# Kernel optimization log

Measured on AMD Instinct MI355X. Metric: run time of the kernel, lower is better.

## Reference

```python
import jax, jax.numpy as jnp
import numpy as np
from jax import lax

N, C, M = 512, 81, 28
NMS_THRESH = 0.5
EPS = 1e-4


def setup_inputs() -> dict:
    key = jax.random.key(0)
    k1, k2, k3, k4 = jax.random.split(key, 4)
    return {
        "left_logits": jax.random.normal(k1, (N, C, M, M), dtype=jnp.float32),
        "right_logits": jax.random.normal(k2, (N, C, M, M), dtype=jnp.float32),
        "scores": jax.random.uniform(k3, (N,), dtype=jnp.float32),
        "labels": jax.random.randint(k4, (N,), 0, C),
    }


def mask_nms_keep(probs, scores, thresh):
    # probs: [N, M, M] float mask probabilities; greedy suppression in score order.
    n = probs.shape[0]
    order = jnp.argsort(-scores)
    P = probs[order].reshape(n, -1)                  # [N, M*M] sorted by score desc
    inter = P @ P.T                                   # pairwise sum(mask_i * mask_j)
    u = P.sum(-1)                                     # per-mask area (numerator mask only)
    iou = inter / (u[:, None] + EPS)                  # asymmetric IoU as in mask_iou()
    upper = jnp.triu(jnp.ones((n, n), dtype=bool), 1) # j > i

    def body(i, suppressed):
        sup_row = (~suppressed[i]) & upper[i] & (iou[i] >= thresh)
        return suppressed | sup_row

    suppressed = lax.fori_loop(0, n, body, jnp.zeros(n, dtype=bool))
    keep_sorted = ~suppressed
    # map back to original detection order
    return jnp.zeros(n, dtype=bool).at[order].set(keep_sorted)


def reference(left_logits, right_logits, scores, labels):
    idx = jnp.arange(left_logits.shape[0])
    # full-tensor sigmoid then per-class gather, as in the original module
    left_prob = jax.nn.sigmoid(left_logits)[idx, labels][:, None]    # [N,1,M,M]
    right_prob = jax.nn.sigmoid(right_logits)[idx, labels][:, None]  # [N,1,M,M]

    # filter_empty: both sides must have nonzero mask mass
    valid = (left_prob[:, 0].sum((-1, -2)) > 0) & (right_prob[:, 0].sum((-1, -2)) > 0)

    left_keep = mask_nms_keep(left_prob[:, 0], scores, NMS_THRESH)
    right_keep = mask_nms_keep(right_prob[:, 0], scores, NMS_THRESH)
    keep = valid & left_keep & right_keep  # intersection of left/right NMS keeps

    probs = jnp.stack([left_prob, right_prob], axis=0)  # [2,N,1,M,M]
    return probs, keep
```

## Files before the change

### kernel.cpp

```cpp
#include <hip/hip_runtime.h>
#include <math.h>

#define NDET 512
#define NCLS 81
#define MM   784
#define PROBS_ELEMS (2 * NDET * MM)
#define NMS_TH 0.5
#define EPS_D  1e-4
#define SDD 114


__global__ __launch_bounds__(256) void k12_fused(
    const float* __restrict__ left, const float* __restrict__ right,
    const float* __restrict__ scores, const int* __restrict__ labels,
    float* __restrict__ out, double* __restrict__ u, int* __restrict__ order) {
  if (blockIdx.x == 256) {
    __shared__ float sk[NDET];
    __shared__ int   si[NDET];
    int t = threadIdx.x;
    for (int e = t; e < NDET; e += 256) { sk[e] = scores[e]; si[e] = e; }
    __syncthreads();
    for (int k = 2; k <= NDET; k <<= 1) {
      for (int j = k >> 1; j > 0; j >>= 1) {
        for (int e = t; e < NDET; e += 256) {
          int p = e ^ j;
          if (p > e) {
            bool dir = ((e & k) == 0);
            float sa = sk[e], sb = sk[p];
            int ia = si[e], ib = si[p];
            bool aBeforeB = (sa > sb) || (sa == sb && ia < ib);
            bool doSwap = dir ? (!aBeforeB) : aBeforeB;
            if (doSwap) { sk[e] = sb; si[e] = ib; sk[p] = sa; si[p] = ia; }
          }
        }
        __syncthreads();
      }
    }
    for (int e = t; e < NDET; e += 256) order[e] = si[e];
    return;
  }

  int wv = threadIdx.x >> 6;
  int lane = threadIdx.x & 63;
  int m = (blockIdx.x << 2) | wv;
  int s = m >> 9;
  int n = m & 511;
  const float* src = (s == 0) ? left : right;
  int lab = labels[n];
  const float4* in4 = (const float4*)(src + ((size_t)n * NCLS + lab) * MM);
  float4* out4 = (float4*)(out + ((size_t)s * NDET + n) * MM);
  double local = 0.0;
  for (int i = lane; i < MM / 4; i += 64) {
    float4 v = in4[i];
    float4 r;
    r.x = 1.0f / (1.0f + expf(-v.x));
    r.y = 1.0f / (1.0f + expf(-v.y));
    r.z = 1.0f / (1.0f + expf(-v.z));
    r.w = 1.0f / (1.0f + expf(-v.w));
    out4[i] = r;
    local += (double)r.x + (double)r.y + (double)r.z + (double)r.w;
  }
#pragma unroll
  for (int off = 32; off > 0; off >>= 1)
    local += __shfl_down(local, off, 64);
  if (lane == 0) u[s * NDET + n] = local;
}

__global__ __launch_bounds__(256) void k3_iou(
    const float* __restrict__ P,
    const double* __restrict__ u,
    const int* __restrict__ order,
    unsigned int* __restrict__ bits32) {
  int bi = blockIdx.x;
  int s = bi / 136;
  int tri = bi % 136;
  int ti = 0, rem = tri;
  while (rem >= 16 - ti) { rem -= 16 - ti; ti++; }
  int tj = ti + rem;

  __shared__ __align__(16) double Asd[32][SDD];
  __shared__ __align__(16) double Bsd[32][SDD];
  __shared__ int oi[32], oj[32];
  __shared__ double den[32];

  int t = threadIdx.x;
  if (t < 32) {
    int r = order[ti * 32 + t];
    oi[t] = r;
    den[t] = u[s * NDET + r] + EPS_D;
    oj[t] = order[tj * 32 + t];
  }
  __syncthreads();

  const float* Pside = P + (size_t)s * NDET * MM;
  int cx = t & 15;
  int ry = t >> 4;
  double a00 = 0.0, a01 = 0.0, a10 = 0.0, a11 = 0.0;

  for (int kc = 0; kc < 7; kc++) {
    int k0 = kc * 112;
    for (int e = t; e < 32 * 28; e += 256) {
      int r = e / 28;
      int c4 = e - r * 28;
      float4 va = *(const float4*)&Pside[(size_t)oi[r] * MM + k0 + 4 * c4];
      float4 vb = *(const float4*)&Pside[(size_t)oj[r] * MM + k0 + 4 * c4];
      double2 a0; a0.x = (double)va.x; a0.y = (double)va.y;
      double2 a1; a1.x = (double)va.z; a1.y = (double)va.w;
      double2 b0; b0.x = (double)vb.x; b0.y = (double)vb.y;
      double2 b1; b1.x = (double)vb.z; b1.y = (double)vb.w;
      *(double2*)&Asd[r][4 * c4]     = a0;
      *(double2*)&Asd[r][4 * c4 + 2] = a1;
      *(double2*)&Bsd[r][4 * c4]     = b0;
      *(double2*)&Bsd[r][4 * c4 + 2] = b1;
    }
    __syncthreads();
    for (int kp = 0; kp < 56; kp++) {
      double2 fa0 = *(const double2*)&Asd[ry][2 * kp];
      double2 fa1 = *(const double2*)&Asd[ry + 16][2 * kp];
      double2 fb0 = *(const double2*)&Bsd[cx][2 * kp];
      double2 fb1 = *(const double2*)&Bsd[cx + 16][2 * kp];
      a00 += fa0.x * fb0.x; a00 += fa0.y * fb0.y;
      a01 += fa0.x * fb1.x; a01 += fa0.y * fb1.y;
      a10 += fa1.x * fb0.x; a10 += fa1.y * fb0.y;
      a11 += fa1.x * fb1.x; a11 += fa1.y * fb1.y;
    }
    __syncthreads();
  }

  bool p00 = (a00 / den[ry]      >= NMS_TH);
  bool p01 = (a01 / den[ry]      >= NMS_TH);
  bool p10 = (a10 / den[ry + 16] >= NMS_TH);
  bool p11 = (a11 / den[ry + 16] >= NMS_TH);
  unsigned long long bl0 = __ballot(p00);
  unsigned long long bh0 = __ballot(p01);
  unsigned long long bl1 = __ballot(p10);
  unsigned long long bh1 = __ballot(p11);
  int q = ry & 3;
  if (cx == 0) {
    unsigned m0 = (unsigned)((bl0 >> (16 * q)) & 0xffffull) |
                  ((unsigned)((bh0 >> (16 * q)) & 0xffffull) << 16);
    unsigned m1 = (unsigned)((bl1 >> (16 * q)) & 0xffffull) |
                  ((unsigned)((bh1 >> (16 * q)) & 0xffffull) << 16);
    bits32[((size_t)s * NDET + ti * 32 + ry) * 16 + tj] = m0;
    bits32[((size_t)s * NDET + ti * 32 + ry + 16) * 16 + tj] = m1;
  }
}

__global__ __launch_bounds__(512) void k4_greedy(
    const unsigned long long* __restrict__ bits,
    const int* __restrict__ order,
    const double* __restrict__ u,
    float* __restrict__ outKeep) {
  __shared__ unsigned long long B[2 * NDET * 8];
  __shared__ unsigned char keepO[2 * NDET];
  int t = threadIdx.x;

  for (int e = t; e < 2 * NDET * 8; e += 512) {
    unsigned long long w = bits[e];
    int g = e & 7;
    int i = (e >> 3) & 511;
    int gi = i >> 6;
    if (g < gi) {
      w = 0ull;
    } else if (g == gi) {
      int li = i & 63;
      w = (li == 63) ? 0ull : (w & (~0ull << (li + 1)));
    }
    B[e] = w;
  }
  __syncthreads();

  int wv = t >> 6;
  int lane = t & 63;
  if (wv < 2) {
    int s = wv;
    const unsigned long long* Bside = B + (size_t)s * NDET * 8;
    unsigned long long S0 = 0, S1 = 0, S2 = 0, S3 = 0,
                       S4 = 0, S5 = 0, S6 = 0, S7 = 0;

#define GROUP(G, SG, ORS)                                              \
    for (int li = 0; li < 64; li++) {                                  \
      unsigned act = (unsigned)((SG >> li) & 1ull);                    \
      if (__builtin_amdgcn_readfirstlane(act) == 0) {                  \
        const unsigned long long* row = Bside + ((((G) << 6) | li) << 3); \
        ORS                                                            \
      }                                                                \
    }
    GROUP(0, S0, { S0 |= row[0]; S1 |= row[1]; S2 |= row[2]; S3 |= row[3];
                   S4 |= row[4]; S5 |= row[5]; S6 |= row[6]; S7 |= row[7]; })
    GROUP(1, S1, { S1 |= row[1]; S2 |= row[2]; S3 |= row[3];
                   S4 |= row[4]; S5 |= row[5]; S6 |= row[6]; S7 |= row[7]; })
    GROUP(2, S2, { S2 |= row[2]; S3 |= row[3];
                   S4 |= row[4]; S5 |= row[5]; S6 |= row[6]; S7 |= row[7]; })
    GROUP(3, S3, { S3 |= row[3];
                   S4 |= row[4]; S5 |= row[5]; S6 |= row[6]; S7 |= row[7]; })
    GROUP(4, S4, { S4 |= row[4]; S5 |= row[5]; S6 |= row[6]; S7 |= row[7]; })
    GROUP(5, S5, { S5 |= row[5]; S6 |= row[6]; S7 |= row[7]; })
    GROUP(6, S6, { S6 |= row[6]; S7 |= row[7]; })
    GROUP(7, S7, { S7 |= row[7]; })
#undef GROUP

    unsigned long long Sarr[8] = {S0, S1, S2, S3, S4, S5, S6, S7};
#pragma unroll
    for (int g = 0; g < 8; g++) {
      int c = (g << 6) | lane;
      keepO[s * NDET + order[c]] =
          (unsigned char)(((Sarr[g] >> lane) & 1ull) ^ 1ull);
    }
  }
  __syncthreads();

  if (t < NDET) {
    bool valid = (u[t] > 0.0) && (u[NDET + t] > 0.0);
    outKeep[t] = (valid && keepO[t] && keepO[NDET + t]) ? 1.0f : 0.0f;
  }
}

extern "C" void kernel_launch(void* const* d_in, const int* in_sizes, int n_in,
                              void* d_out, int out_size, void* d_ws, size_t ws_size,
                              hipStream_t stream) {
  const float* left   = (const float*)d_in[0];
  const float* right  = (const float*)d_in[1];
  const float* scores = (const float*)d_in[2];
  const int*   labels = (const int*)d_in[3];
  float* out = (float*)d_out;

  char* ws = (char*)d_ws;
  double* u                = (double*)(ws + 0);
  int* order               = (int*)(ws + 8192);
  unsigned int* bits32     = (unsigned int*)(ws + 16384);
  unsigned long long* bits = (unsigned long long*)(ws + 16384);

  k12_fused<<<257, 256, 0, stream>>>(left, right, scores, labels, out, u, order);
  k3_iou<<<272, 256, 0, stream>>>(out, u, order, bits32);
  k4_greedy<<<1, 512, 0, stream>>>(bits, order, u, out + PROBS_ELEMS);
}
```

Measured before the change: 292.7 us.

## Use FP64 MFMA for pairwise mask IoU with register-prefetched float tiles

Replaces the scalar FP64 FMA inner product in the IoU kernel with the 16x16x4 FP64 MFMA instruction, one 16x16 quadrant per wavefront. Tiles are now stored as float in LDS (halving LDS traffic) and converted to double when loaded, and the next K-chunk is prefetched into registers while the current one computes. A dummy MFMA is used to discover the output lane layout, and the threshold test is rewritten as a comparison against half the denominator, removing a double division. This adds complexity and relies on the MFMA output mapping. Summing the two accumulators changes the order of summation, which could flip borderline IoU comparisons.

```diff
diff --git a/kernel.cpp b/kernel.cpp
--- a/kernel.cpp
+++ b/kernel.cpp
@@ -7,7 +7,9 @@
 #define PROBS_ELEMS (2 * NDET * MM)
 #define NMS_TH 0.5
 #define EPS_D  1e-4
-#define SDD 114
+#define SD 116
+
+typedef double dbl4 __attribute__((ext_vector_type(4)));
 
 
 __global__ __launch_bounds__(256) void k12_fused(
@@ -78,71 +80,94 @@
   while (rem >= 16 - ti) { rem -= 16 - ti; ti++; }
   int tj = ti + rem;
 
-  __shared__ __align__(16) double Asd[32][SDD];
-  __shared__ __align__(16) double Bsd[32][SDD];
+  __shared__ __align__(16) float As[32][SD];
+  __shared__ __align__(16) float Bs[32][SD];
   __shared__ int oi[32], oj[32];
-  __shared__ double den[32];
+  __shared__ double den05[32];
+  __shared__ unsigned char pred[32][32];
 
   int t = threadIdx.x;
   if (t < 32) {
     int r = order[ti * 32 + t];
     oi[t] = r;
-    den[t] = u[s * NDET + r] + EPS_D;
+    den05[t] = 0.5 * (u[s * NDET + r] + EPS_D);
     oj[t] = order[tj * 32 + t];
   }
   __syncthreads();
 
   const float* Pside = P + (size_t)s * NDET * MM;
-  int cx = t & 15;
-  int ry = t >> 4;
-  double a00 = 0.0, a01 = 0.0, a10 = 0.0, a11 = 0.0;
+
+  const float4* gsrc[7];
+  float* ldst[7];
+#pragma unroll
+  for (int i = 0; i < 7; i++) {
+    int idx = t + 256 * i;
+    int ab = (idx >= 896);
+    int idc = ab ? (idx - 896) : idx;
+    int r = idc / 28;
+    int c4 = idc - r * 28;
+    int o = ab ? oj[r] : oi[r];
+    gsrc[i] = (const float4*)(Pside + (size_t)o * MM) + c4;
+    ldst[i] = ab ? &Bs[r][4 * c4] : &As[r][4 * c4];
+  }
+
+  float4 pf[7];
+#pragma unroll
+  for (int i = 0; i < 7; i++) pf[i] = gsrc[i][0];
+
+  int wv = t >> 6;
+  int lane = t & 63;
+  int qi = (wv >> 1) & 1;
+  int qj = wv & 1;
+  int fr = lane & 15;
+  int fk = lane >> 4;
+  const float* aF = &As[qi * 16 + fr][fk];
+  const float* bF = &Bs[qj * 16 + fr][fk];
+
+  double ap = (fk == 0) ? 1.0 : (fk == 1) ? (double)fr : 0.0;
+  double bp = (fk == 0) ? (double)fr : (fk == 1) ? 16.0 : 0.0;
+  dbl4 dp = {0.0, 0.0, 0.0, 0.0};
+  dp = __builtin_amdgcn_mfma_f64_16x16x4f64(ap, bp, dp, 0, 0, 0);
+
+  dbl4 acc0 = {0.0, 0.0, 0.0, 0.0};
+  dbl4 acc1 = {0.0, 0.0, 0.0, 0.0};
 
   for (int kc = 0; kc < 7; kc++) {
-    int k0 = kc * 112;
-    for (int e = t; e < 32 * 28; e += 256) {
-      int r = e / 28;
-      int c4 = e - r * 28;
-      float4 va = *(const float4*)&Pside[(size_t)oi[r] * MM + k0 + 4 * c4];
-      float4 vb = *(const float4*)&Pside[(size_t)oj[r] * MM + k0 + 4 * c4];
-      double2 a0; a0.x = (double)va.x; a0.y = (double)va.y;
-      double2 a1; a1.x = (double)va.z; a1.y = (double)va.w;
-      double2 b0; b0.x = (double)vb.x; b0.y = (double)vb.y;
-      double2 b1; b1.x = (double)vb.z; b1.y = (double)vb.w;
-      *(double2*)&Asd[r][4 * c4]     = a0;
-      *(double2*)&Asd[r][4 * c4 + 2] = a1;
-      *(double2*)&Bsd[r][4 * c4]     = b0;
-      *(double2*)&Bsd[r][4 * c4 + 2] = b1;
-    }
+#pragma unroll
+    for (int i = 0; i < 7; i++) *(float4*)ldst[i] = pf[i];
     __syncthreads();
-    for (int kp = 0; kp < 56; kp++) {
-      double2 fa0 = *(const double2*)&Asd[ry][2 * kp];
-      double2 fa1 = *(const double2*)&Asd[ry + 16][2 * kp];
-      double2 fb0 = *(const double2*)&Bsd[cx][2 * kp];
-      double2 fb1 = *(const double2*)&Bsd[cx + 16][2 * kp];
-      a00 += fa0.x * fb0.x; a00 += fa0.y * fb0.y;
-      a01 += fa0.x * fb1.x; a01 += fa0.y * fb1.y;
-      a10 += fa1.x * fb0.x; a10 += fa1.y * fb0.y;
-      a11 += fa1.x * fb1.x; a11 += fa1.y * fb1.y;
+    if (kc < 6) {
+#pragma unroll
+      for (int i = 0; i < 7; i++) pf[i] = gsrc[i][(kc + 1) * 28];
+    }
+#pragma unroll
+    for (int st = 0; st < 28; st += 2) {
+      double a0 = (double)aF[st * 4];
+      double b0 = (double)bF[st * 4];
+      acc0 = __builtin_amdgcn_mfma_f64_16x16x4f64(a0, b0, acc0, 0, 0, 0);
+      double a1 = (double)aF[(st + 1) * 4];
+      double b1 = (double)bF[(st + 1) * 4];
+      acc1 = __builtin_amdgcn_mfma_f64_16x16x4f64(a1, b1, acc1, 0, 0, 0);
     }
     __syncthreads();
   }
 
-  bool p00 = (a00 / den[ry]      >= NMS_TH);
-  bool p01 = (a01 / den[ry]      >= NMS_TH);
-  bool p10 = (a10 / den[ry + 16] >= NMS_TH);
-  bool p11 = (a11 / den[ry + 16] >= NMS_TH);
-  unsigned long long bl0 = __ballot(p00);
-  unsigned long long bh0 = __ballot(p01);
-  unsigned long long bl1 = __ballot(p10);
-  unsigned long long bh1 = __ballot(p11);
-  int q = ry & 3;
-  if (cx == 0) {
-    unsigned m0 = (unsigned)((bl0 >> (16 * q)) & 0xffffull) |
-                  ((unsigned)((bh0 >> (16 * q)) & 0xffffull) << 16);
-    unsigned m1 = (unsigned)((bl1 >> (16 * q)) & 0xffffull) |
-                  ((unsigned)((bh1 >> (16 * q)) & 0xffffull) << 16);
-    bits32[((size_t)s * NDET + ti * 32 + ry) * 16 + tj] = m0;
-    bits32[((size_t)s * NDET + ti * 32 + ry + 16) * 16 + tj] = m1;
+#pragma unroll
+  for (int r = 0; r < 4; r++) {
+    int code = (int)dp[r];
+    int di = code >> 4;
+    int dj = code & 15;
+    double v = acc0[r] + acc1[r];
+    bool p = (v >= den05[qi * 16 + di]);
+    pred[qi * 16 + di][qj * 16 + dj] = p ? 1 : 0;
+  }
+  __syncthreads();
+
+  if (t < 32) {
+    unsigned m = 0;
+#pragma unroll
+    for (int c = 0; c < 32; c++) m |= ((unsigned)pred[t][c]) << c;
+    bits32[((size_t)s * NDET + ti * 32 + t) * 16 + tj] = m;
   }
 }
 
```

After: 296.6 us. Within noise of the previous version (+1.3%).
